# Kernel tuning notes

Hardware: AMD Instinct MI355X
Metric: run time of the kernel (lower is better)

Reference implementation:

```python
import jax, jax.numpy as jnp
import numpy as np

B, T, N, M = 128, 128, 128, 256  # batch, timesteps, driving series, hidden size


def setup_inputs() -> dict:
    key = jax.random.key(0)
    ks = jax.random.split(key, 8)
    def p(k, shape, fan):
        return jax.random.normal(k, shape, jnp.float32) / np.float32(np.sqrt(fan))
    X = jax.random.normal(ks[0], (B, T, N), jnp.float32)
    h0 = jnp.zeros((B, M), jnp.float32)
    s0 = jnp.zeros((B, M), jnp.float32)
    Wx = p(ks[1], (N, 4 * M), N)           # LSTM input kernel (gates i,f,g,o)
    Wh = p(ks[2], (M, 4 * M), M)           # LSTM recurrent kernel
    b = jnp.zeros((4 * M,), jnp.float32)
    Wd = p(ks[3], (2 * M, T), 2 * M)       # attention W: Dense(T) on [h;s]
    bW = jnp.zeros((T,), jnp.float32)
    Ud = p(ks[4], (T, T), T)               # attention U: Dense(T) on X^T
    bU = jnp.zeros((T,), jnp.float32)
    vd = p(ks[5], (T, 1), T)               # attention v: Dense(1)
    bv = jnp.zeros((1,), jnp.float32)
    return {"X": X, "h0": h0, "s0": s0, "Wx": Wx, "Wh": Wh, "b": b,
            "Wd": Wd, "bW": bW, "Ud": Ud, "bU": bU, "vd": vd, "bv": bv}


def reference(X, h0, s0, Wx, Wh, b, Wd, bW, Ud, bU, vd, bv):
    m = h0.shape[-1]
    # U(Permute(X)) is time-invariant: precompute once. (B,N,T)
    UX = jnp.einsum('btn,tu->bnu', X, Ud) + bU

    def lstm_cell(h, c, x_t):
        z = x_t @ Wx + h @ Wh + b                      # (B,4M)
        i, f, g, o = jnp.split(z, 4, axis=-1)
        i = jax.nn.sigmoid(i)
        f = jax.nn.sigmoid(f)
        g = jnp.tanh(g)
        o = jax.nn.sigmoid(o)
        c = f * c + i * g
        h = o * jnp.tanh(c)
        return h, c

    def step(carry, x_t):
        h, c = carry
        h, c = lstm_cell(h, c, x_t)                    # (B,M),(B,M)
        hs = jnp.concatenate([h, c], axis=-1)          # (B,2M)
        w = hs @ Wd + bW                               # (B,T), broadcast over N
        e = jnp.tanh(w[:, None, :] + UX) @ vd          # (B,N,1)
        alpha = jax.nn.softmax(e[..., 0] + bv[0], axis=-1)  # softmax over N
        return (h, c), alpha

    (_, _), alphas = jax.lax.scan(step, (h0, s0), jnp.swapaxes(X, 0, 1))
    # alphas: (T,B,N) -> (B,T,N); x_tilde = alpha_t (.) x_t
    return X * jnp.swapaxes(alphas, 0, 1)
```

## Files before the change

kernel.cpp:

```cpp
#include <hip/hip_runtime.h>
#include <hip/hip_fp16.h>

#define Bc 128
#define Tc 128
#define Nc 128
#define Mc 256
#define G4 1024

typedef _Float16 half8 __attribute__((ext_vector_type(8)));
typedef float f32x4 __attribute__((ext_vector_type(4)));
typedef unsigned u32x4 __attribute__((ext_vector_type(4)));

__device__ __forceinline__ float frcp(float x) {
#if __has_builtin(__builtin_amdgcn_rcpf)
  return __builtin_amdgcn_rcpf(x);
#else
  return 1.f / x;
#endif
}
__device__ __forceinline__ float fsig(float x) { return frcp(1.f + __expf(-x)); }
__device__ __forceinline__ float ftanh(float x) {
  float t = __expf(2.f * x);
  return 1.f - 2.f * frcp(t + 1.f);
}

#define LDX4CC(dst, ptr, OFF) \
  asm volatile("global_load_dwordx4 %0, %1, off offset:" #OFF " sc0 sc1" \
               : "=v"(dst) : "v"(ptr))
#define LDX4P(dst, ptr, OFF) \
  asm volatile("global_load_dwordx4 %0, %1, off offset:" #OFF \
               : "=v"(dst) : "v"(ptr))
#define ATOMSW(ptr, v_) \
  asm volatile("global_atomic_swap %0, %1, off" :: "v"(ptr), "v"(v_) : "memory")
#define STDWP(ptr, v_) \
  asm volatile("global_store_dword %0, %1, off" :: "v"(ptr), "v"(v_) : "memory")
#define VMCNT0 do { asm volatile("s_waitcnt vmcnt(0)" ::: "memory"); \
                    __builtin_amdgcn_sched_barrier(0); } while (0)

__global__ void k_prep(const float* __restrict__ Wh, const float* __restrict__ Wx,
                       const float* __restrict__ X, const float* __restrict__ h0,
                       __half* __restrict__ wht, __half* __restrict__ wxt,
                       __half* __restrict__ xtp, unsigned* __restrict__ hx2,
                       unsigned* __restrict__ flags) {
  int bid = blockIdx.x;
  if (bid < 512) {
    int i = bid * 256 + threadIdx.x;
    int jt = i >> 11;
    int rem = i & 2047;
    int kt = rem >> 8;
    int rem2 = rem & 255;
    int lane = rem2 >> 2;
    int r2 = rem2 & 3;
    int jp = jt * 16 + (lane & 15);
    int g = jp & 3, mcol = jp >> 2;
    int j = g * 256 + mcol;
    int mk0 = kt * 32 + (lane >> 4) * 8 + r2;
    wht[(size_t)i * 2]     = __float2half(Wh[(size_t)mk0 * G4 + j]);
    wht[(size_t)i * 2 + 1] = __float2half(Wh[(size_t)(mk0 + 4) * G4 + j]);
  } else if (bid < 768) {
    int i = (bid - 512) * 256 + threadIdx.x;
    int jt = i >> 10;
    int rem = i & 1023;
    int kt = rem >> 8;
    int rem2 = rem & 255;
    int lane = rem2 >> 2;
    int r2 = rem2 & 3;
    int jp = jt * 16 + (lane & 15);
    int g = jp & 3, mcol = jp >> 2;
    int j = g * 256 + mcol;
    int n0 = kt * 32 + (lane >> 4) * 8 + 2 * r2;
    wxt[(size_t)i * 2]     = __float2half(Wx[(size_t)n0 * G4 + j]);
    wxt[(size_t)i * 2 + 1] = __float2half(Wx[(size_t)(n0 + 1) * G4 + j]);
  } else if (bid < 832) {
    int idx = (bid - 768) * 256 + threadIdx.x;
    int b = idx >> 7, i = idx & 127;
    int a = i >> 2, d = i & 3;
    unsigned lo = __half_as_ushort(__float2half(h0[(size_t)b * Mc + 8 * a + d]));
    unsigned hi = __half_as_ushort(__float2half(h0[(size_t)b * Mc + 8 * a + d + 4]));
    hx2[idx] = ~(lo | (hi << 16));
  } else if (bid < 9024) {
    int idx = (bid - 832) * 256 + threadIdx.x;
    hx2[16384 + idx] = 0u;
  } else if (bid < 13120) {
    int i = (bid - 9024) * 256 + threadIdx.x;
    int t = i >> 13;
    int rem = i & 8191;
    int b = rem >> 6;
    int rem2 = rem & 63;
    int kt = rem2 >> 4;
    int r = rem2 & 15;
    int lg = r >> 2, r2 = r & 3;
    int n0 = kt * 32 + lg * 8 + 2 * r2;
    const float* xr = X + ((size_t)b * Tc + t) * Nc;
    xtp[(size_t)i * 2]     = __float2half(xr[n0]);
    xtp[(size_t)i * 2 + 1] = __float2half(xr[n0 + 1]);
  } else {
    for (int i = threadIdx.x; i < 16544; i += 256) flags[i] = 0u;
  }
}

__global__ void k_ux(const float* __restrict__ X, const float* __restrict__ Ud,
                     const float* __restrict__ bU, float* __restrict__ PX) {
  __shared__ float Xl[Tc][Nc];
  int b = blockIdx.x;
  const float* Xb = X + (size_t)b * Tc * Nc;
  for (int i = threadIdx.x; i < Tc * Nc; i += 256) Xl[i >> 7][i & 127] = Xb[i];
  __syncthreads();
  int n = threadIdx.x & 127;
  int uh = __builtin_amdgcn_readfirstlane(threadIdx.x >> 7);
  for (int u0 = uh * 64; u0 < uh * 64 + 64; u0 += 8) {
    float acc[8];
#pragma unroll
    for (int i = 0; i < 8; i++) acc[i] = 0.f;
    for (int tt = 0; tt < Tc; ++tt) {
      float xv = Xl[tt][n];
#pragma unroll
      for (int i = 0; i < 8; i++) acc[i] += xv * Ud[tt * Tc + u0 + i];
    }
#pragma unroll
    for (int i = 0; i < 8; i++)
      PX[((size_t)b * Tc + (u0 + i)) * Nc + n] = __expf(2.f * (acc[i] + bU[u0 + i]));
  }
}

template <bool FAST>
__device__ __forceinline__ void scan_body(
    const __half* __restrict__ wht, const __half* __restrict__ wxt,
    const __half* __restrict__ xtp,
    unsigned* __restrict__ hx2, __half* __restrict__ cx,
    const float* __restrict__ s0, const float* __restrict__ bb,
    unsigned* __restrict__ flags,
    int q, int grp, int tid, int lane, int lg, int b, int jt0, int m0) {
  half8 A0[8], A1[8];
#pragma unroll
  for (int kt = 0; kt < 8; ++kt) {
    A0[kt] = *(const half8*)(wht + ((size_t)(jt0 * 8 + kt) * 64 + lane) * 8);
    A1[kt] = *(const half8*)(wht + ((size_t)((jt0 + 1) * 8 + kt) * 64 + lane) * 8);
  }
  half8 Ax0[4], Ax1[4];
#pragma unroll
  for (int kt = 0; kt < 4; ++kt) {
    Ax0[kt] = *(const half8*)(wxt + ((size_t)(jt0 * 4 + kt) * 64 + lane) * 8);
    Ax1[kt] = *(const half8*)(wxt + ((size_t)((jt0 + 1) * 4 + kt) * 64 + lane) * 8);
  }
  f32x4 binit0, binit1;
  binit0[0] = bb[m0];       binit0[1] = bb[256 + m0];
  binit0[2] = bb[512 + m0]; binit0[3] = bb[768 + m0];
  binit1[0] = bb[m0 + 4];       binit1[1] = bb[256 + m0 + 4];
  binit1[2] = bb[512 + m0 + 4]; binit1[3] = bb[768 + m0 + 4];

  float c0 = s0[(size_t)b * Mc + m0];
  float c1 = s0[(size_t)b * Mc + m0 + 4];

  const char* hq = (const char*)hx2 + ((size_t)b * 128 + lg * 4) * 4;
  char*       hs = (char*)hx2 + ((size_t)16384 + b * 128 + jt0 * 2 + lg) * 4;
  const char* xt = (const char*)xtp + (size_t)b * 256 + lg * 16;
  __half*      cq = cx + (size_t)b * Mc;
  unsigned* flgp = flags + (size_t)grp * 129 * 16;

  f32x4 braw[8];
  f32x4 bx0, bx1, bx2, bx3;

#pragma unroll 1
  for (int t = 0; t < 128; ++t) {
    asm volatile("" : "+v"(A0[0]), "+v"(A0[1]), "+v"(A0[2]), "+v"(A0[3]),
                      "+v"(A0[4]), "+v"(A0[5]), "+v"(A0[6]), "+v"(A0[7]));
    asm volatile("" : "+v"(A1[0]), "+v"(A1[1]), "+v"(A1[2]), "+v"(A1[3]),
                      "+v"(A1[4]), "+v"(A1[5]), "+v"(A1[6]), "+v"(A1[7]));
    asm volatile("" : "+v"(Ax0[0]), "+v"(Ax0[1]), "+v"(Ax0[2]), "+v"(Ax0[3]),
                      "+v"(Ax1[0]), "+v"(Ax1[1]), "+v"(Ax1[2]), "+v"(Ax1[3]),
                      "+v"(binit0), "+v"(binit1));

    LDX4P(bx0, xt, 0); LDX4P(bx1, xt, 64); LDX4P(bx2, xt, 128); LDX4P(bx3, xt, 192);

    if (FAST) {
      if (t > 0) {
        unsigned ret = 0u;
#pragma unroll 1
        do {
          if (lane == 0)
            asm volatile("global_atomic_or %0, %1, %2, off sc0\n\t"
                         "s_waitcnt vmcnt(0)"
                         : "=v"(ret) : "v"(flgp + t * 16), "v"(0u) : "memory");
          ret = __builtin_amdgcn_readfirstlane(ret);
        } while (ret < 4u);
        __builtin_amdgcn_sched_barrier(0);
      }
      LDX4P(braw[0], hq, 0);   LDX4P(braw[1], hq, 64);
      LDX4P(braw[2], hq, 128); LDX4P(braw[3], hq, 192);
      LDX4P(braw[4], hq, 256); LDX4P(braw[5], hq, 320);
      LDX4P(braw[6], hq, 384); LDX4P(braw[7], hq, 448);
      VMCNT0;
    } else {
      LDX4CC(braw[0], hq, 0);   LDX4CC(braw[1], hq, 64);
      LDX4CC(braw[2], hq, 128); LDX4CC(braw[3], hq, 192);
      LDX4CC(braw[4], hq, 256); LDX4CC(braw[5], hq, 320);
      LDX4CC(braw[6], hq, 384); LDX4CC(braw[7], hq, 448);
      for (;;) {
        VMCNT0;
        unsigned mn = 0xFFFFFFFFu;
#pragma unroll
        for (int kt = 0; kt < 8; ++kt) {
          u32x4 u = __builtin_bit_cast(u32x4, braw[kt]);
          mn = min(mn, min(min(u.x, u.y), min(u.z, u.w)));
        }
        if (__builtin_expect(mn != 0u, 1)) break;
        LDX4CC(braw[0], hq, 0);   LDX4CC(braw[1], hq, 64);
        LDX4CC(braw[2], hq, 128); LDX4CC(braw[3], hq, 192);
        LDX4CC(braw[4], hq, 256); LDX4CC(braw[5], hq, 320);
        LDX4CC(braw[6], hq, 384); LDX4CC(braw[7], hq, 448);
      }
    }

    f32x4 acc0 = binit0, acc1 = binit1;
    {
      half8 B0 = __builtin_bit_cast(half8, bx0);
      half8 B1 = __builtin_bit_cast(half8, bx1);
      half8 B2 = __builtin_bit_cast(half8, bx2);
      half8 B3 = __builtin_bit_cast(half8, bx3);
      acc0 = __builtin_amdgcn_mfma_f32_16x16x32_f16(Ax0[0], B0, acc0, 0, 0, 0);
      acc1 = __builtin_amdgcn_mfma_f32_16x16x32_f16(Ax1[0], B0, acc1, 0, 0, 0);
      acc0 = __builtin_amdgcn_mfma_f32_16x16x32_f16(Ax0[1], B1, acc0, 0, 0, 0);
      acc1 = __builtin_amdgcn_mfma_f32_16x16x32_f16(Ax1[1], B1, acc1, 0, 0, 0);
      acc0 = __builtin_amdgcn_mfma_f32_16x16x32_f16(Ax0[2], B2, acc0, 0, 0, 0);
      acc1 = __builtin_amdgcn_mfma_f32_16x16x32_f16(Ax1[2], B2, acc1, 0, 0, 0);
      acc0 = __builtin_amdgcn_mfma_f32_16x16x32_f16(Ax0[3], B3, acc0, 0, 0, 0);
      acc1 = __builtin_amdgcn_mfma_f32_16x16x32_f16(Ax1[3], B3, acc1, 0, 0, 0);
    }
#pragma unroll
    for (int kt = 0; kt < 8; ++kt) {
      u32x4 u = ~__builtin_bit_cast(u32x4, braw[kt]);
      half8 Bf = __builtin_bit_cast(half8, u);
      acc0 = __builtin_amdgcn_mfma_f32_16x16x32_f16(A0[kt], Bf, acc0, 0, 0, 0);
      acc1 = __builtin_amdgcn_mfma_f32_16x16x32_f16(A1[kt], Bf, acc1, 0, 0, 0);
    }
    float i0 = fsig(acc0[0]), f0 = fsig(acc0[1]);
    float g0 = ftanh(acc0[2]), o0 = fsig(acc0[3]);
    c0 = f0 * c0 + i0 * g0;
    float h0v = o0 * ftanh(c0);
    float i1 = fsig(acc1[0]), f1 = fsig(acc1[1]);
    float g1 = ftanh(acc1[2]), o1 = fsig(acc1[3]);
    c1 = f1 * c1 + i1 * g1;
    float h1v = o1 * ftanh(c1);

    unsigned pk = (unsigned)__half_as_ushort(__float2half(h0v)) |
                  ((unsigned)__half_as_ushort(__float2half(h1v)) << 16);
    if (FAST) {
      STDWP(hs, ~pk);
      VMCNT0;
      __syncthreads();
      if (tid == 0)
        asm volatile("global_atomic_add %0, %1, off"
                     :: "v"(flgp + (t + 1) * 16), "v"(1u) : "memory");
      cq[m0]     = __float2half(c0);
      cq[m0 + 4] = __float2half(c1);
    } else {
      ATOMSW(hs, ~pk);
      cq[m0]     = __float2half(c0);
      cq[m0 + 4] = __float2half(c1);
    }

    hq += 65536; hs += 65536; xt += 32768; cq += Bc * Mc;
  }
}

__global__ __launch_bounds__(512, 1)
void k_scan(const __half* __restrict__ wht, const __half* __restrict__ wxt,
            const __half* __restrict__ xtp,
            unsigned* __restrict__ hx2, __half* __restrict__ cx,
            const float* __restrict__ s0, const float* __restrict__ bb,
            unsigned* __restrict__ flags) {
  int bid = blockIdx.x;
  int q = bid >> 3, grp = bid & 7;
  int tid = threadIdx.x;
  int lane = tid & 63;
  int lb = lane & 15, lg = lane >> 4;
  int b = grp * 16 + lb;
  int jt0 = q * 16 + (tid >> 6) * 2;
  int m0 = jt0 * 4 + lg;

  unsigned* xcdtab = flags + 16512;
  __shared__ int s_fast;
  if (tid == 0) {
    unsigned xcd;
    asm volatile("s_getreg_b32 %0, hwreg(HW_REG_XCC_ID)" : "=s"(xcd));
    asm volatile("global_store_dword %0, %1, off sc0 sc1"
                 :: "v"(xcdtab + bid), "v"(xcd + 1u) : "memory");
    unsigned ref = 0; int fast = 1;
#pragma unroll 1
    for (int k = 0; k < 4; ++k) {
      unsigned v;
      do {
        asm volatile("global_load_dword %0, %1, off sc0 sc1\n\t"
                     "s_waitcnt vmcnt(0)"
                     : "=v"(v) : "v"(xcdtab + (k * 8 + grp)) : "memory");
      } while (v == 0u);
      if (k == 0) ref = v; else fast &= (v == ref) ? 1 : 0;
    }
    s_fast = fast;
  }
  __syncthreads();

  if (s_fast)
    scan_body<true>(wht, wxt, xtp, hx2, cx, s0, bb, flags, q, grp, tid, lane, lg, b, jt0, m0);
  else
    scan_body<false>(wht, wxt, xtp, hx2, cx, s0, bb, flags, q, grp, tid, lane, lg, b, jt0, m0);
}

__global__ void k_wall2(const unsigned* __restrict__ Hxu, const __half2* __restrict__ Cx2,
                        const float* __restrict__ Wd, const float* __restrict__ bW,
                        float* __restrict__ Wall) {
  int r0 = blockIdx.x * 32;
  int wv = __builtin_amdgcn_readfirstlane(threadIdx.x >> 6);
  int lane = threadIdx.x & 63;
  int u2 = lane * 2;
  int rbase = r0 + wv * 8;
  float acc[8][2];
#pragma unroll
  for (int i = 0; i < 8; i++) { acc[i][0] = 0.f; acc[i][1] = 0.f; }
#pragma unroll 2
  for (int k2 = 0; k2 < 128; ++k2) {
    int m_lo = 8 * (k2 >> 2) + (k2 & 3);
    float2 wh0 = *(const float2*)(Wd + (size_t)m_lo * Tc + u2);
    float2 wh1 = *(const float2*)(Wd + (size_t)(m_lo + 4) * Tc + u2);
    float2 wc0 = *(const float2*)(Wd + (size_t)(Mc + 2 * k2) * Tc + u2);
    float2 wc1 = *(const float2*)(Wd + (size_t)(Mc + 2 * k2 + 1) * Tc + u2);
#pragma unroll
    for (int i = 0; i < 8; i++) {
      unsigned hraw = ~Hxu[(size_t)(rbase + i) * 128 + 16384 + k2];
      __half2 hv = __builtin_bit_cast(__half2, hraw);
      __half2 cv = Cx2[(size_t)(rbase + i) * 128 + k2];
      float hlo = __low2float(hv), hhi = __high2float(hv);
      float clo = __low2float(cv), chi = __high2float(cv);
      acc[i][0] += hlo * wh0.x + hhi * wh1.x + clo * wc0.x + chi * wc1.x;
      acc[i][1] += hlo * wh0.y + hhi * wh1.y + clo * wc0.y + chi * wc1.y;
    }
  }
  float bw0 = bW[u2], bw1 = bW[u2 + 1];
#pragma unroll
  for (int i = 0; i < 8; i++) {
    float2 o; o.x = acc[i][0] + bw0; o.y = acc[i][1] + bw1;
    *(float2*)(Wall + (size_t)(rbase + i) * Tc + u2) = o;
  }
}

__global__ void k_attn(const float* __restrict__ Wall, const float* __restrict__ PX,
                       const float* __restrict__ vd, const float* __restrict__ X,
                       float* __restrict__ out) {
  __shared__ float4 av[Nc];
  __shared__ float v2s[Nc];
  __shared__ float red[2][8];
  int b = blockIdx.x & 127, tq = blockIdx.x >> 7;
  int n = threadIdx.x;
  int wv = n >> 6;
  float4 a;
  a.x = __expf(2.f * Wall[((size_t)(tq * 4 + 0) * Bc + b) * Tc + n]);
  a.y = __expf(2.f * Wall[((size_t)(tq * 4 + 1) * Bc + b) * Tc + n]);
  a.z = __expf(2.f * Wall[((size_t)(tq * 4 + 2) * Bc + b) * Tc + n]);
  a.w = __expf(2.f * Wall[((size_t)(tq * 4 + 3) * Bc + b) * Tc + n]);
  av[n] = a;
  v2s[n] = -2.f * vd[n];
  __syncthreads();
  const float* Pb = PX + (size_t)b * Tc * Nc;
  float e0 = 0.f, e1 = 0.f, e2 = 0.f, e3 = 0.f;
#pragma unroll 4
  for (int u = 0; u < Tc; ++u) {
    float P = Pb[(size_t)u * Nc + n];
    float4 au = av[u];
    float v2 = v2s[u];
    e0 = fmaf(v2, frcp(fmaf(au.x, P, 1.f)), e0);
    e1 = fmaf(v2, frcp(fmaf(au.y, P, 1.f)), e1);
    e2 = fmaf(v2, frcp(fmaf(au.z, P, 1.f)), e2);
    e3 = fmaf(v2, frcp(fmaf(au.w, P, 1.f)), e3);
  }
  float m0 = e0, m1 = e1, m2 = e2, m3 = e3;
#pragma unroll
  for (int off = 32; off > 0; off >>= 1) {
    m0 = fmaxf(m0, __shfl_xor(m0, off));
    m1 = fmaxf(m1, __shfl_xor(m1, off));
    m2 = fmaxf(m2, __shfl_xor(m2, off));
    m3 = fmaxf(m3, __shfl_xor(m3, off));
  }
  if ((n & 63) == 0) {
    red[wv][0] = m0; red[wv][1] = m1; red[wv][2] = m2; red[wv][3] = m3;
  }
  __syncthreads();
  m0 = fmaxf(red[0][0], red[1][0]);
  m1 = fmaxf(red[0][1], red[1][1]);
  m2 = fmaxf(red[0][2], red[1][2]);
  m3 = fmaxf(red[0][3], red[1][3]);
  float x0 = __expf(e0 - m0);
  float x1 = __expf(e1 - m1);
  float x2 = __expf(e2 - m2);
  float x3 = __expf(e3 - m3);
  float s0 = x0, s1 = x1, s2 = x2, s3 = x3;
#pragma unroll
  for (int off = 32; off > 0; off >>= 1) {
    s0 += __shfl_xor(s0, off);
    s1 += __shfl_xor(s1, off);
    s2 += __shfl_xor(s2, off);
    s3 += __shfl_xor(s3, off);
  }
  if ((n & 63) == 0) {
    red[wv][4] = s0; red[wv][5] = s1; red[wv][6] = s2; red[wv][7] = s3;
  }
  __syncthreads();
  s0 = red[0][4] + red[1][4];
  s1 = red[0][5] + red[1][5];
  s2 = red[0][6] + red[1][6];
  s3 = red[0][7] + red[1][7];
  size_t xi0 = ((size_t)b * Tc + tq * 4) * Nc + n;
  out[xi0]            = X[xi0]            * (x0 * frcp(s0));
  out[xi0 + Nc]       = X[xi0 + Nc]       * (x1 * frcp(s1));
  out[xi0 + 2 * Nc]   = X[xi0 + 2 * Nc]   * (x2 * frcp(s2));
  out[xi0 + 3 * Nc]   = X[xi0 + 3 * Nc]   * (x3 * frcp(s3));
}

extern "C" void kernel_launch(void* const* d_in, const int* in_sizes, int n_in,
                              void* d_out, int out_size, void* d_ws, size_t ws_size,
                              hipStream_t stream) {
  (void)in_sizes; (void)n_in; (void)out_size; (void)ws_size;
  const float* X  = (const float*)d_in[0];
  const float* h0 = (const float*)d_in[1];
  const float* s0 = (const float*)d_in[2];
  const float* Wx = (const float*)d_in[3];
  const float* Wh = (const float*)d_in[4];
  const float* bb = (const float*)d_in[5];
  const float* Wd = (const float*)d_in[6];
  const float* bW = (const float*)d_in[7];
  const float* Ud = (const float*)d_in[8];
  const float* bU = (const float*)d_in[9];
  const float* vd = (const float*)d_in[10];
  float* out = (float*)d_out;
  float* ws = (float*)d_ws;

  float* PX       = ws;
  unsigned* hx2   = (unsigned*)(PX + 2097152);
  __half* cx      = (__half*)(hx2 + 129 * 16384);
  float* Wall     = (float*)(cx + 128 * 32768);
  __half* wht     = (__half*)(Wall + 2097152);
  __half* wxt     = wht + 262144;
  __half* xtp     = wxt + 131072;
  unsigned* flags = (unsigned*)(xtp + 2097152);

  k_prep<<<13121, 256, 0, stream>>>(Wh, Wx, X, h0, wht, wxt, xtp, hx2, flags);
  k_ux<<<Bc, 256, 0, stream>>>(X, Ud, bU, PX);
  k_scan<<<32, 512, 0, stream>>>(wht, wxt, xtp, hx2, cx, s0, bb, flags);
  k_wall2<<<(Tc * Bc) / 32, 256, 0, stream>>>(hx2, (const __half2*)cx, Wd, bW, Wall);
  k_attn<<<Bc * 32, 128, 0, stream>>>(Wall, PX, vd, X, out);
}
```

Before: 644.9 us.

## Fuse UX precompute into scan launch, fold Wall into attention, prefetch x_t

```diff
diff --git a/kernel.cpp b/kernel.cpp
--- a/kernel.cpp
+++ b/kernel.cpp
@@ -35,6 +35,8 @@
 #define STDWP(ptr, v_) \
   asm volatile("global_store_dword %0, %1, off" :: "v"(ptr), "v"(v_) : "memory")
 #define VMCNT0 do { asm volatile("s_waitcnt vmcnt(0)" ::: "memory"); \
+                    __builtin_amdgcn_sched_barrier(0); } while (0)
+#define VMCNT4 do { asm volatile("s_waitcnt vmcnt(4)" ::: "memory"); \
                     __builtin_amdgcn_sched_barrier(0); } while (0)
 
 __global__ void k_prep(const float* __restrict__ Wh, const float* __restrict__ Wx,
@@ -78,11 +80,13 @@
     unsigned lo = __half_as_ushort(__float2half(h0[(size_t)b * Mc + 8 * a + d]));
     unsigned hi = __half_as_ushort(__float2half(h0[(size_t)b * Mc + 8 * a + d + 4]));
     hx2[idx] = ~(lo | (hi << 16));
-  } else if (bid < 9024) {
+  } else if (bid < 1344) {
     int idx = (bid - 832) * 256 + threadIdx.x;
-    hx2[16384 + idx] = 0u;
-  } else if (bid < 13120) {
-    int i = (bid - 9024) * 256 + threadIdx.x;
+    u32x4 z = {0u, 0u, 0u, 0u};
+    u32x4* p = (u32x4*)(hx2 + 16384) + (size_t)idx * 4;
+    p[0] = z; p[1] = z; p[2] = z; p[3] = z;
+  } else if (bid < 5440) {
+    int i = (bid - 1344) * 256 + threadIdx.x;
     int t = i >> 13;
     int rem = i & 8191;
     int b = rem >> 6;
@@ -99,30 +103,6 @@
   }
 }
 
-__global__ void k_ux(const float* __restrict__ X, const float* __restrict__ Ud,
-                     const float* __restrict__ bU, float* __restrict__ PX) {
-  __shared__ float Xl[Tc][Nc];
-  int b = blockIdx.x;
-  const float* Xb = X + (size_t)b * Tc * Nc;
-  for (int i = threadIdx.x; i < Tc * Nc; i += 256) Xl[i >> 7][i & 127] = Xb[i];
-  __syncthreads();
-  int n = threadIdx.x & 127;
-  int uh = __builtin_amdgcn_readfirstlane(threadIdx.x >> 7);
-  for (int u0 = uh * 64; u0 < uh * 64 + 64; u0 += 8) {
-    float acc[8];
-#pragma unroll
-    for (int i = 0; i < 8; i++) acc[i] = 0.f;
-    for (int tt = 0; tt < Tc; ++tt) {
-      float xv = Xl[tt][n];
-#pragma unroll
-      for (int i = 0; i < 8; i++) acc[i] += xv * Ud[tt * Tc + u0 + i];
-    }
-#pragma unroll
-    for (int i = 0; i < 8; i++)
-      PX[((size_t)b * Tc + (u0 + i)) * Nc + n] = __expf(2.f * (acc[i] + bU[u0 + i]));
-  }
-}
-
 template <bool FAST>
 __device__ __forceinline__ void scan_body(
     const __half* __restrict__ wht, const __half* __restrict__ wxt,
@@ -159,7 +139,13 @@
   unsigned* flgp = flags + (size_t)grp * 129 * 16;
 
   f32x4 braw[8];
-  f32x4 bx0, bx1, bx2, bx3;
+  f32x4 bxA0, bxA1, bxA2, bxA3;
+  f32x4 bxB0, bxB1, bxB2, bxB3;
+
+  asm volatile("s_waitcnt vmcnt(0)" ::: "memory");
+  __builtin_amdgcn_sched_barrier(0);
+  LDX4P(bxA0, xt, 0); LDX4P(bxA1, xt, 64);
+  LDX4P(bxA2, xt, 128); LDX4P(bxA3, xt, 192);
 
 #pragma unroll 1
   for (int t = 0; t < 128; ++t) {
@@ -170,8 +156,6 @@
     asm volatile("" : "+v"(Ax0[0]), "+v"(Ax0[1]), "+v"(Ax0[2]), "+v"(Ax0[3]),
                       "+v"(Ax1[0]), "+v"(Ax1[1]), "+v"(Ax1[2]), "+v"(Ax1[3]),
                       "+v"(binit0), "+v"(binit1));
-
-    LDX4P(bx0, xt, 0); LDX4P(bx1, xt, 64); LDX4P(bx2, xt, 128); LDX4P(bx3, xt, 192);
 
     if (FAST) {
       if (t > 0) {
@@ -214,10 +198,10 @@
 
     f32x4 acc0 = binit0, acc1 = binit1;
     {
-      half8 B0 = __builtin_bit_cast(half8, bx0);
-      half8 B1 = __builtin_bit_cast(half8, bx1);
-      half8 B2 = __builtin_bit_cast(half8, bx2);
-      half8 B3 = __builtin_bit_cast(half8, bx3);
+      half8 B0 = __builtin_bit_cast(half8, bxA0);
+      half8 B1 = __builtin_bit_cast(half8, bxA1);
+      half8 B2 = __builtin_bit_cast(half8, bxA2);
+      half8 B3 = __builtin_bit_cast(half8, bxA3);
       acc0 = __builtin_amdgcn_mfma_f32_16x16x32_f16(Ax0[0], B0, acc0, 0, 0, 0);
       acc1 = __builtin_amdgcn_mfma_f32_16x16x32_f16(Ax1[0], B0, acc1, 0, 0, 0);
       acc0 = __builtin_amdgcn_mfma_f32_16x16x32_f16(Ax0[1], B1, acc0, 0, 0, 0);
@@ -247,17 +231,30 @@
                   ((unsigned)__half_as_ushort(__float2half(h1v)) << 16);
     if (FAST) {
       STDWP(hs, ~pk);
-      VMCNT0;
+      if (t < 127) {
+        const char* xtn = xt + 32768;
+        LDX4P(bxB0, xtn, 0); LDX4P(bxB1, xtn, 64);
+        LDX4P(bxB2, xtn, 128); LDX4P(bxB3, xtn, 192);
+        VMCNT4;
+      } else {
+        VMCNT0;
+      }
       __syncthreads();
       if (tid == 0)
         asm volatile("global_atomic_add %0, %1, off"
                      :: "v"(flgp + (t + 1) * 16), "v"(1u) : "memory");
       cq[m0]     = __float2half(c0);
       cq[m0 + 4] = __float2half(c1);
+      bxA0 = bxB0; bxA1 = bxB1; bxA2 = bxB2; bxA3 = bxB3;
     } else {
       ATOMSW(hs, ~pk);
       cq[m0]     = __float2half(c0);
       cq[m0 + 4] = __float2half(c1);
+      if (t < 127) {
+        const char* xtn = xt + 32768;
+        LDX4P(bxA0, xtn, 0); LDX4P(bxA1, xtn, 64);
+        LDX4P(bxA2, xtn, 128); LDX4P(bxA3, xtn, 192);
+      }
     }
 
     hq += 65536; hs += 65536; xt += 32768; cq += Bc * Mc;
@@ -269,10 +266,38 @@
             const __half* __restrict__ xtp,
             unsigned* __restrict__ hx2, __half* __restrict__ cx,
             const float* __restrict__ s0, const float* __restrict__ bb,
-            unsigned* __restrict__ flags) {
+            unsigned* __restrict__ flags,
+            const float* __restrict__ X, const float* __restrict__ Ud,
+            const float* __restrict__ bU, float* __restrict__ PX) {
+  __shared__ float Xl[Tc][Nc];
+  __shared__ int s_fast;
   int bid = blockIdx.x;
+  int tid = threadIdx.x;
+
+  if (bid >= 32) {
+    int b = bid - 32;
+    const float* Xb = X + (size_t)b * Tc * Nc;
+    for (int i = tid; i < Tc * Nc; i += 512) Xl[i >> 7][i & 127] = Xb[i];
+    __syncthreads();
+    int n = tid & 127;
+    int uh = __builtin_amdgcn_readfirstlane(tid >> 7);
+    for (int u0 = uh * 32; u0 < uh * 32 + 32; u0 += 8) {
+      float acc[8];
+#pragma unroll
+      for (int i = 0; i < 8; i++) acc[i] = 0.f;
+      for (int tt = 0; tt < Tc; ++tt) {
+        float xv = Xl[tt][n];
+#pragma unroll
+        for (int i = 0; i < 8; i++) acc[i] += xv * Ud[tt * Tc + u0 + i];
+      }
+#pragma unroll
+      for (int i = 0; i < 8; i++)
+        PX[((size_t)b * Tc + (u0 + i)) * Nc + n] = __expf(2.f * (acc[i] + bU[u0 + i]));
+    }
+    return;
+  }
+
   int q = bid >> 3, grp = bid & 7;
-  int tid = threadIdx.x;
   int lane = tid & 63;
   int lb = lane & 15, lg = lane >> 4;
   int b = grp * 16 + lb;
@@ -280,7 +305,6 @@
   int m0 = jt0 * 4 + lg;
 
   unsigned* xcdtab = flags + 16512;
-  __shared__ int s_fast;
   if (tid == 0) {
     unsigned xcd;
     asm volatile("s_getreg_b32 %0, hwreg(HW_REG_XCC_ID)" : "=s"(xcd));
@@ -307,59 +331,63 @@
     scan_body<false>(wht, wxt, xtp, hx2, cx, s0, bb, flags, q, grp, tid, lane, lg, b, jt0, m0);
 }
 
-__global__ void k_wall2(const unsigned* __restrict__ Hxu, const __half2* __restrict__ Cx2,
-                        const float* __restrict__ Wd, const float* __restrict__ bW,
-                        float* __restrict__ Wall) {
-  int r0 = blockIdx.x * 32;
-  int wv = __builtin_amdgcn_readfirstlane(threadIdx.x >> 6);
-  int lane = threadIdx.x & 63;
-  int u2 = lane * 2;
-  int rbase = r0 + wv * 8;
-  float acc[8][2];
-#pragma unroll
-  for (int i = 0; i < 8; i++) { acc[i][0] = 0.f; acc[i][1] = 0.f; }
-#pragma unroll 2
-  for (int k2 = 0; k2 < 128; ++k2) {
-    int m_lo = 8 * (k2 >> 2) + (k2 & 3);
-    float2 wh0 = *(const float2*)(Wd + (size_t)m_lo * Tc + u2);
-    float2 wh1 = *(const float2*)(Wd + (size_t)(m_lo + 4) * Tc + u2);
-    float2 wc0 = *(const float2*)(Wd + (size_t)(Mc + 2 * k2) * Tc + u2);
-    float2 wc1 = *(const float2*)(Wd + (size_t)(Mc + 2 * k2 + 1) * Tc + u2);
-#pragma unroll
-    for (int i = 0; i < 8; i++) {
-      unsigned hraw = ~Hxu[(size_t)(rbase + i) * 128 + 16384 + k2];
-      __half2 hv = __builtin_bit_cast(__half2, hraw);
-      __half2 cv = Cx2[(size_t)(rbase + i) * 128 + k2];
-      float hlo = __low2float(hv), hhi = __high2float(hv);
-      float clo = __low2float(cv), chi = __high2float(cv);
-      acc[i][0] += hlo * wh0.x + hhi * wh1.x + clo * wc0.x + chi * wc1.x;
-      acc[i][1] += hlo * wh0.y + hhi * wh1.y + clo * wc0.y + chi * wc1.y;
-    }
-  }
-  float bw0 = bW[u2], bw1 = bW[u2 + 1];
-#pragma unroll
-  for (int i = 0; i < 8; i++) {
-    float2 o; o.x = acc[i][0] + bw0; o.y = acc[i][1] + bw1;
-    *(float2*)(Wall + (size_t)(rbase + i) * Tc + u2) = o;
-  }
-}
-
-__global__ void k_attn(const float* __restrict__ Wall, const float* __restrict__ PX,
-                       const float* __restrict__ vd, const float* __restrict__ X,
-                       float* __restrict__ out) {
+__global__ void k_attn(const unsigned* __restrict__ Hxu, const unsigned* __restrict__ Cxu,
+                       const float* __restrict__ Wd, const float* __restrict__ bW,
+                       const float* __restrict__ PX, const float* __restrict__ vd,
+                       const float* __restrict__ X, float* __restrict__ out) {
+  __shared__ unsigned hl[4][Nc];
+  __shared__ unsigned cl[4][Nc];
   __shared__ float4 av[Nc];
   __shared__ float v2s[Nc];
   __shared__ float red[2][8];
   int b = blockIdx.x & 127, tq = blockIdx.x >> 7;
   int n = threadIdx.x;
   int wv = n >> 6;
+#pragma unroll
+  for (int k = 0; k < 4; ++k) {
+    int t = tq * 4 + k;
+    hl[k][n] = Hxu[(size_t)(t + 1) * 16384 + b * 128 + n];
+    cl[k][n] = Cxu[((size_t)t * 128 + b) * 128 + n];
+  }
+  v2s[n] = -2.f * vd[n];
+  __syncthreads();
+  float a0 = bW[n], a1 = bW[n], a2 = bW[n], a3 = bW[n];
+#pragma unroll 2
+  for (int k2 = 0; k2 < 128; ++k2) {
+    int m_lo = 8 * (k2 >> 2) + (k2 & 3);
+    float wh0 = Wd[(size_t)m_lo * Tc + n];
+    float wh1 = Wd[(size_t)(m_lo + 4) * Tc + n];
+    float wc0 = Wd[(size_t)(Mc + 2 * k2) * Tc + n];
+    float wc1 = Wd[(size_t)(Mc + 2 * k2 + 1) * Tc + n];
+    {
+      __half2 hv = __builtin_bit_cast(__half2, ~hl[0][k2]);
+      __half2 cv = __builtin_bit_cast(__half2, cl[0][k2]);
+      a0 += __low2float(hv) * wh0 + __high2float(hv) * wh1 +
+            __low2float(cv) * wc0 + __high2float(cv) * wc1;
+    }
+    {
+      __half2 hv = __builtin_bit_cast(__half2, ~hl[1][k2]);
+      __half2 cv = __builtin_bit_cast(__half2, cl[1][k2]);
+      a1 += __low2float(hv) * wh0 + __high2float(hv) * wh1 +
+            __low2float(cv) * wc0 + __high2float(cv) * wc1;
+    }
+    {
+      __half2 hv = __builtin_bit_cast(__half2, ~hl[2][k2]);
+      __half2 cv = __builtin_bit_cast(__half2, cl[2][k2]);
+      a2 += __low2float(hv) * wh0 + __high2float(hv) * wh1 +
+            __low2float(cv) * wc0 + __high2float(cv) * wc1;
+    }
+    {
+      __half2 hv = __builtin_bit_cast(__half2, ~hl[3][k2]);
+      __half2 cv = __builtin_bit_cast(__half2, cl[3][k2]);
+      a3 += __low2float(hv) * wh0 + __high2float(hv) * wh1 +
+            __low2float(cv) * wc0 + __high2float(cv) * wc1;
+    }
+  }
   float4 a;
-  a.x = __expf(2.f * Wall[((size_t)(tq * 4 + 0) * Bc + b) * Tc + n]);
-  a.y = __expf(2.f * Wall[((size_t)(tq * 4 + 1) * Bc + b) * Tc + n]);
-  a.z = __expf(2.f * Wall[((size_t)(tq * 4 + 2) * Bc + b) * Tc + n]);
-  a.w = __expf(2.f * Wall[((size_t)(tq * 4 + 3) * Bc + b) * Tc + n]);
+  a.x = __expf(2.f * a0); a.y = __expf(2.f * a1);
+  a.z = __expf(2.f * a2); a.w = __expf(2.f * a3);
   av[n] = a;
-  v2s[n] = -2.f * vd[n];
   __syncthreads();
   const float* Pb = PX + (size_t)b * Tc * Nc;
   float e0 = 0.f, e1 = 0.f, e2 = 0.f, e3 = 0.f;
@@ -436,16 +464,14 @@
 
   float* PX       = ws;
   unsigned* hx2   = (unsigned*)(PX + 2097152);
-  __half* cx      = (__half*)(hx2 + 129 * 16384);
-  float* Wall     = (float*)(cx + 128 * 32768);
-  __half* wht     = (__half*)(Wall + 2097152);
+  unsigned* cxu   = hx2 + 129 * 16384;
+  __half* wht     = (__half*)(cxu + 128 * 16384);
   __half* wxt     = wht + 262144;
   __half* xtp     = wxt + 131072;
   unsigned* flags = (unsigned*)(xtp + 2097152);
 
-  k_prep<<<13121, 256, 0, stream>>>(Wh, Wx, X, h0, wht, wxt, xtp, hx2, flags);
-  k_ux<<<Bc, 256, 0, stream>>>(X, Ud, bU, PX);
-  k_scan<<<32, 512, 0, stream>>>(wht, wxt, xtp, hx2, cx, s0, bb, flags);
-  k_wall2<<<(Tc * Bc) / 32, 256, 0, stream>>>(hx2, (const __half2*)cx, Wd, bW, Wall);
-  k_attn<<<Bc * 32, 128, 0, stream>>>(Wall, PX, vd, X, out);
-}
+  k_prep<<<5441, 256, 0, stream>>>(Wh, Wx, X, h0, wht, wxt, xtp, hx2, flags);
+  k_scan<<<160, 512, 0, stream>>>(wht, wxt, xtp, hx2, (__half*)cxu, s0, bb, flags,
+                                  X, Ud, bU, PX);
+  k_attn<<<Bc * 32, 128, 0, stream>>>(hx2, cxu, Wd, bW, PX, vd, X, out);
+}
```

Measured after the change: 580.7 us. -9.9%, faster.
